# Kernel tuning notes

Measured on AMD Instinct MI355X. Metric: run time of the kernel, lower is better.

The kernel has to match this reference:

```python
import jax, jax.numpy as jnp
import numpy as np

H = 1024   # HIDDEN_DIM
V = 15000  # VOCAB_SIZE
L = 2      # NUM_LAYERS
E = 4      # experts per block
B, S = 32, 2048


def rmsnorm(x, w, eps=1e-6):
    return x * jax.lax.rsqrt(jnp.mean(x * x, axis=-1, keepdims=True) + eps) * w


def setup_inputs() -> dict:
    key = jax.random.key(0)
    ks = jax.random.split(key, 8)
    windows = jax.random.randint(ks[0], (B, S), 0, V, dtype=jnp.int32)
    hemis = jax.random.randint(ks[1], (B,), 0, 2, dtype=jnp.int32)
    experts = jax.random.randint(ks[2], (B,), 0, E, dtype=jnp.int32)
    emb = jax.random.normal(ks[3], (V, H), dtype=jnp.float32) * 0.02
    norm1_w = jnp.ones((L, H), dtype=jnp.float32)
    decay_logit = jnp.full((L, H), 2.0, dtype=jnp.float32)  # torch init: ones*2.0
    norm2_w = jnp.ones((L, H), dtype=jnp.float32)
    # expert weights, torch Linear layout [out, in] per expert: [L, E, H, H]
    Wexp = jax.random.normal(ks[4], (L, E, H, H), dtype=jnp.float32) * 0.02
    final_norm_w = jnp.ones((H,), dtype=jnp.float32)
    lm_head = jax.random.normal(ks[5], (V, H), dtype=jnp.float32) * 0.02
    return dict(windows=windows, hemis=hemis, experts=experts, emb=emb,
                norm1_w=norm1_w, decay_logit=decay_logit, norm2_w=norm2_w,
                Wexp=Wexp, final_norm_w=final_norm_w, lm_head=lm_head)


def reference(windows, hemis, experts, emb, norm1_w, decay_logit, norm2_w,
              Wexp, final_norm_w, lm_head):
    del hemis  # only used for router loss when targets are given (inference path)
    x = emb[windows]  # [B,S,H]
    onehot = jax.nn.one_hot(experts, E, dtype=x.dtype)  # [B,E]
    for l in range(L):
        xn = rmsnorm(x, norm1_w[l])
        decay = jax.nn.sigmoid(decay_logit[l])  # [H]

        def step(state, xt):
            s = state * decay + xt * (1.0 - decay)
            return s, s

        init = jnp.zeros((x.shape[0], H), dtype=x.dtype)
        _, states = jax.lax.scan(step, init, jnp.swapaxes(xn, 0, 1))  # [S,B,H]
        x = x + jnp.swapaxes(states, 0, 1)
        pool = rmsnorm(x, norm2_w[l])[:, -1, :]  # [B,H]
        # all 4 expert FFNs on the pooled state, then select by expert id
        out_all = jax.nn.relu(jnp.einsum('bh,edh->ebd', pool, Wexp[l]))  # [E,B,H]
        out = jnp.einsum('be,ebh->bh', onehot, out_all)  # [B,H]
        x = x + out[:, None, :]
    final_state = rmsnorm(x[:, -1, :], final_norm_w)
    logits = final_state @ lm_head.T  # [B,V]
    return logits
```

## Files before the change

### kernel.cpp

```cpp
#include <hip/hip_runtime.h>
#include <cstddef>
#include <cstdint>

#define H 1024
#define V 15000
#define NE 4
#define B 32
#define S 2048
#define EPS 1e-6f
#define CH 16
#define T0 128
#define NVB 469
#define LGRID 1024

typedef unsigned short u16;

__device__ __forceinline__ float wave_sum(float x) {
#pragma unroll
  for (int off = 32; off > 0; off >>= 1) x += __shfl_down(x, off);
  return x;
}

__device__ __forceinline__ float bf2f(u16 u) {
  union { uint32_t i; float f; } x;
  x.i = ((uint32_t)u) << 16;
  return x.f;
}

__device__ __forceinline__ u16 f2bf(float f) {
  union { float f; uint32_t i; } x;
  x.f = f;
  const uint32_t u = x.i;
  return (u16)((u + 0x7FFFu + ((u >> 16) & 1u)) >> 16);
}

__device__ __forceinline__ void pin4(float4& v) {
  asm volatile("" : "+v"(v.x), "+v"(v.y), "+v"(v.z), "+v"(v.w));
}

__global__ __launch_bounds__(256) void k_vocab(const float* __restrict__ emb,
                                               float* __restrict__ invr1,
                                               u16* __restrict__ embh) {
  const int gw = (blockIdx.x * blockDim.x + threadIdx.x) >> 6;
  const int lane = threadIdx.x & 63;
  if (gw >= V) return;
  const float4* row = (const float4*)(emb + (size_t)gw * H);
  float s = 0.f;
#pragma unroll
  for (int j = 0; j < 4; ++j) {
    const float4 f = row[lane + 64 * j];
    s += f.x * f.x + f.y * f.y + f.z * f.z + f.w * f.w;
    if (embh) {
      ushort4 h4;
      h4.x = f2bf(f.x); h4.y = f2bf(f.y); h4.z = f2bf(f.z); h4.w = f2bf(f.w);
      ((ushort4*)(embh + (size_t)gw * H))[lane + 64 * j] = h4;
    }
  }
  s = wave_sum(s);
  if (lane == 0) invr1[gw] = rsqrtf(s * (1.f / H) + EPS);
}

__global__ void k_bucket(const int* __restrict__ experts,
                         int* __restrict__ elist, int* __restrict__ ecnt) {
  if (threadIdx.x == 0 && blockIdx.x == 0) {
    int c[NE] = {0, 0, 0, 0};
    for (int b = 0; b < B; ++b) {
      const int e = experts[b];
      elist[e * B + c[e]] = b;
      c[e]++;
    }
    for (int e = 0; e < NE; ++e) ecnt[e] = c[e];
  }
}

template <int BF>
__global__ __launch_bounds__(1024, 8) void k_scanA(
    const int* __restrict__ windows, const float* __restrict__ emb,
    const u16* __restrict__ embh, const float* __restrict__ norm1_w,
    const float* __restrict__ decay_logit, const float* __restrict__ invr1,
    float* __restrict__ local1) {
  __shared__ int tok_l[T0];
  __shared__ float iv_l[T0];
  const int b = blockIdx.x / CH, c = blockIdx.x % CH;
  const int h = threadIdx.x;
  if (h < T0) {
    const int tok = windows[b * S + c * T0 + h];
    tok_l[h] = tok << 10;
    iv_l[h] = invr1[tok];
  }
  const float d1 = 1.f / (1.f + expf(-decay_logit[h]));
  const float gw = norm1_w[h] * (1.f - d1);
  __syncthreads();
  float s = 0.f;
  for (int t0 = 0; t0 < T0; t0 += 8) {
    float e[8], cv[8];
#pragma unroll
    for (int k = 0; k < 8; ++k) {
      if constexpr (BF)
        e[k] = bf2f(embh[(size_t)tok_l[t0 + k] + h]);
      else
        e[k] = emb[(size_t)tok_l[t0 + k] + h];
      cv[k] = iv_l[t0 + k] * gw;
    }
#pragma unroll
    for (int k = 0; k < 8; ++k) s = s * d1 + e[k] * cv[k];
  }
  local1[(size_t)(b * CH + c) * H + h] = s;
}

__global__ __launch_bounds__(1024) void k_scanB(
    const int* __restrict__ windows, const float* __restrict__ emb,
    const float* __restrict__ decay_logit, const float* __restrict__ local1,
    float* __restrict__ s1start, float* __restrict__ es1,
    float* __restrict__ invp) {
  __shared__ float red[16];
  const int b = blockIdx.x, h = threadIdx.x;
  const float d1 = 1.f / (1.f + expf(-decay_logit[h]));
  float dT = d1;
#pragma unroll
  for (int i = 0; i < 7; ++i) dT *= dT;
  float Sv = 0.f;
  for (int c = 0; c < CH; ++c) {
    const size_t idx = (size_t)(b * CH + c) * H + h;
    s1start[idx] = Sv;
    Sv = dT * Sv + local1[idx];
  }
  const int tl = windows[b * S + S - 1];
  const float v = emb[(size_t)tl * H + h] + Sv;
  es1[b * H + h] = v;
  const float q = wave_sum(v * v);
  if ((h & 63) == 0) red[h >> 6] = q;
  __syncthreads();
  if (h == 0) {
    float t = 0.f;
#pragma unroll
    for (int i = 0; i < 16; ++i) t += red[i];
    invp[b] = rsqrtf(t * (1.f / H) + EPS);
  }
}

__global__ __launch_bounds__(256) void k_expert2(
    const float* __restrict__ src, const float* __restrict__ invp,
    const float* __restrict__ n2w, const float* __restrict__ Wl,
    const int* __restrict__ elist, const int* __restrict__ ecnt,
    float* __restrict__ outp) {
  const int e = blockIdx.x >> 6;
  const int dgrp = blockIdx.x & 63;
  const int cnt = ecnt[e];
  if (cnt == 0) return;
  const int wave = threadIdx.x >> 6, lane = threadIdx.x & 63;
  const float* W = Wl + (size_t)e * H * H;
  const float4* n2w4 = (const float4*)n2w;
#pragma unroll 1
  for (int i = 0; i < 4; ++i) {
    const int dd = dgrp * 16 + wave * 4 + i;
    const float4* wr4 = (const float4*)(W + (size_t)dd * H);
    float4 w4[4];
#pragma unroll
    for (int j = 0; j < 4; ++j) w4[j] = wr4[lane + 64 * j];
#pragma unroll 1
    for (int bi = 0; bi < cnt; ++bi) {
      const int b = elist[e * B + bi];
      const float4* s4 = (const float4*)(src + b * H);
      float s = 0.f;
#pragma unroll
      for (int j = 0; j < 4; ++j) {
        const float4 sv = s4[lane + 64 * j];
        const float4 nv = n2w4[lane + 64 * j];
        s += w4[j].x * sv.x * nv.x + w4[j].y * sv.y * nv.y +
             w4[j].z * sv.z * nv.z + w4[j].w * sv.w * nv.w;
      }
      s = wave_sum(s);
      if (lane == 0) outp[b * H + dd] = fmaxf(s * invp[b], 0.f);
    }
  }
}

template <int BF>
__global__ __launch_bounds__(1024, 8) void k_fuseCD(
    const int* __restrict__ windows, const float* __restrict__ emb,
    const u16* __restrict__ embh, const float* __restrict__ norm1_w,
    const float* __restrict__ decay_logit, const float* __restrict__ invr1,
    const float* __restrict__ s1start, const float* __restrict__ out1,
    float* __restrict__ local2, float* __restrict__ x1last) {
  __shared__ int tok_l[T0];
  __shared__ float iv_l[T0];
  __shared__ float q[16 * H];
  __shared__ float rinv_l[16];
  const int b = blockIdx.x / CH, c = blockIdx.x % CH;
  const int h = threadIdx.x;
  if (h < T0) {
    const int tok = windows[b * S + c * T0 + h];
    tok_l[h] = tok << 10;
    iv_l[h] = invr1[tok];
  }
  const float d1 = 1.f / (1.f + expf(-decay_logit[h]));
  const float g1 = norm1_w[h] * (1.f - d1);
  const float d2 = 1.f / (1.f + expf(-decay_logit[H + h]));
  const float g2 = norm1_w[H + h] * (1.f - d2);
  const float o1 = out1[b * H + h];
  float s1 = s1start[(size_t)(b * CH + c) * H + h];
  __syncthreads();
  const int wv = h >> 6, lane = h & 63;
  float s2 = 0.f;
  for (int sb = 0; sb < T0 / 16; ++sb) {
#pragma unroll
    for (int g = 0; g < 2; ++g) {
      float e[8], cv[8];
#pragma unroll
      for (int k = 0; k < 8; ++k) {
        const int t = sb * 16 + g * 8 + k;
        if constexpr (BF)
          e[k] = bf2f(embh[(size_t)tok_l[t] + h]);
        else
          e[k] = emb[(size_t)tok_l[t] + h];
        cv[k] = iv_l[t] * g1;
      }
#pragma unroll
      for (int k = 0; k < 8; ++k) {
        s1 = s1 * d1 + e[k] * cv[k];
        q[(g * 8 + k) * H + h] = e[k] + s1 + o1;
      }
    }
    __syncthreads();
    const float4* q4 = (const float4*)(q + wv * H);
    float ssum = 0.f;
#pragma unroll
    for (int j = 0; j < 4; ++j) {
      const float4 f = q4[lane + 64 * j];
      ssum += f.x * f.x + f.y * f.y + f.z * f.z + f.w * f.w;
    }
    ssum = wave_sum(ssum);
    if (lane == 0) rinv_l[wv] = rsqrtf(ssum * (1.f / H) + EPS);
    __syncthreads();
#pragma unroll
    for (int g = 0; g < 2; ++g) {
      float xv[8], rc[8];
#pragma unroll
      for (int k = 0; k < 8; ++k) {
        xv[k] = q[(g * 8 + k) * H + h];
        rc[k] = rinv_l[g * 8 + k] * g2;
      }
#pragma unroll
      for (int k = 0; k < 8; ++k) s2 = s2 * d2 + xv[k] * rc[k];
    }
    __syncthreads();
  }
  local2[(size_t)(b * CH + c) * H + h] = s2;
  if (c == CH - 1) x1last[b * H + h] = q[15 * H + h];
}

__global__ __launch_bounds__(1024) void k_scanE(
    const float* __restrict__ decay_logit, const float* __restrict__ local2,
    const float* __restrict__ x1last, float* __restrict__ es2,
    float* __restrict__ invp) {
  __shared__ float red[16];
  const int b = blockIdx.x, h = threadIdx.x;
  const float d2 = 1.f / (1.f + expf(-decay_logit[H + h]));
  float dT = d2;
#pragma unroll
  for (int i = 0; i < 7; ++i) dT *= dT;
  float Sv = 0.f;
  for (int c = 0; c < CH; ++c)
    Sv = dT * Sv + local2[(size_t)(b * CH + c) * H + h];
  const float v = x1last[b * H + h] + Sv;
  es2[b * H + h] = v;
  const float q = wave_sum(v * v);
  if ((h & 63) == 0) red[h >> 6] = q;
  __syncthreads();
  if (h == 0) {
    float t = 0.f;
#pragma unroll
    for (int i = 0; i < 16; ++i) t += red[i];
    invp[32 + b] = rsqrtf(t * (1.f / H) + EPS);
  }
}

__global__ __launch_bounds__(256) void k_fstate(const float* __restrict__ es2,
    const float* __restrict__ out2, const float* __restrict__ fnw,
    float* __restrict__ fst) {
  __shared__ float red[4];
  const int b = blockIdx.x, tid = threadIdx.x;
  float4 x = ((const float4*)(es2 + b * H))[tid];
  const float4 y = ((const float4*)(out2 + b * H))[tid];
  x.x += y.x; x.y += y.y; x.z += y.z; x.w += y.w;
  float s = x.x * x.x + x.y * x.y + x.z * x.z + x.w * x.w;
  s = wave_sum(s);
  if ((tid & 63) == 0) red[tid >> 6] = s;
  __syncthreads();
  const float ir =
      rsqrtf((red[0] + red[1] + red[2] + red[3]) * (1.f / H) + EPS);
  const float4 w = ((const float4*)fnw)[tid];
  float4 o;
  o.x = x.x * ir * w.x; o.y = x.y * ir * w.y;
  o.z = x.z * ir * w.z; o.w = x.w * ir * w.w;
  ((float4*)(fst + b * H))[tid] = o;
}

__global__ __launch_bounds__(256, 4) void k_logits(const float* __restrict__ fst,
    const float* __restrict__ lm, float* __restrict__ part) {
  __shared__ float4 fs4[16 * 128];
  const int hh = blockIdx.x & 1;
  const int bgrp = (blockIdx.x >> 1) & 1;
  const int pblk = blockIdx.x >> 2;
  const int tid = threadIdx.x;
  const int wave = tid >> 6, lane = tid & 63;
  const int sg = lane >> 4;
  const int c = lane & 15;
  for (int j = tid; j < 16 * 128; j += 256) {
    const int bb = j >> 7, q = j & 127;
    fs4[j] = ((const float4*)fst)[(bgrp * 16 + bb) * 256 + hh * 128 + q];
  }
  __syncthreads();
  float* pdst = part + (size_t)hh * B * V + (size_t)bgrp * 16 * V;
#pragma unroll 1
  for (int vblk = pblk; vblk < NVB; vblk += LGRID / 4) {
    const int v0 = vblk * 32 + wave * 8 + sg * 2;
    float4 rv[2][8];
#pragma unroll
    for (int i = 0; i < 2; ++i) {
      int r = v0 + i;
      if (r > V - 1) r = V - 1;
      const float4* rp = (const float4*)(lm + (size_t)r * H) + hh * 128 + c;
#pragma unroll
      for (int jj = 0; jj < 8; ++jj) rv[i][jj] = rp[16 * jj];
    }
#pragma unroll
    for (int i = 0; i < 2; ++i)
#pragma unroll
      for (int jj = 0; jj < 8; ++jj) pin4(rv[i][jj]);
    float acc[2][16];
#pragma unroll
    for (int i = 0; i < 2; ++i)
#pragma unroll
      for (int bb = 0; bb < 16; ++bb) acc[i][bb] = 0.f;
#pragma unroll
    for (int jj = 0; jj < 8; ++jj) {
      const int hoff = c + 16 * jj;
#pragma unroll
      for (int bb = 0; bb < 16; ++bb) {
        const float4 fv = fs4[bb * 128 + hoff];
#pragma unroll
        for (int i = 0; i < 2; ++i) {
          acc[i][bb] += rv[i][jj].x * fv.x + rv[i][jj].y * fv.y +
                        rv[i][jj].z * fv.z + rv[i][jj].w * fv.w;
        }
      }
    }
#pragma unroll
    for (int off = 1; off < 16; off <<= 1)
#pragma unroll
      for (int i = 0; i < 2; ++i)
#pragma unroll
        for (int bb = 0; bb < 16; ++bb)
          acc[i][bb] += __shfl_xor(acc[i][bb], off);
    if (c == 0) {
#pragma unroll
      for (int bb = 0; bb < 16; ++bb)
#pragma unroll
        for (int i = 0; i < 2; ++i) {
          const int r = v0 + i;
          if (r < V) pdst[(size_t)bb * V + r] = acc[i][bb];
        }
    }
  }
}

__global__ __launch_bounds__(256) void k_comb(const float* __restrict__ part,
                                              float* __restrict__ outp) {
  const int i = blockIdx.x * 256 + threadIdx.x;
  if (i < B * V) outp[i] = part[i] + part[B * V + i];
}

extern "C" void kernel_launch(void* const* d_in, const int* in_sizes, int n_in,
                              void* d_out, int out_size, void* d_ws,
                              size_t ws_size, hipStream_t stream) {
  const int* windows = (const int*)d_in[0];
  const int* experts = (const int*)d_in[2];
  const float* emb = (const float*)d_in[3];
  const float* norm1_w = (const float*)d_in[4];
  const float* decay_logit = (const float*)d_in[5];
  const float* norm2_w = (const float*)d_in[6];
  const float* Wexp = (const float*)d_in[7];
  const float* final_norm_w = (const float*)d_in[8];
  const float* lm_head = (const float*)d_in[9];
  float* outp = (float*)d_out;

  float* ws = (float*)d_ws;
  float* invr1 = ws;
  float* local1 = invr1 + 15360;
  float* s1start = local1 + B * CH * H;
  float* local2 = s1start + B * CH * H;
  float* out1 = local2 + B * CH * H;
  float* out2 = out1 + B * H;
  float* es1 = out2 + B * H;
  float* es2 = es1 + B * H;
  float* x1last = es2 + B * H;
  float* fst = x1last + B * H;
  float* invp = fst + B * H;
  int* elist = (int*)(invp + 64);
  int* ecnt = elist + NE * B;
  float* part = local1;
  u16* embh = (u16*)(((uintptr_t)(ecnt + NE) + 255) & ~(uintptr_t)255);
  const size_t need = (size_t)((char*)embh - (char*)d_ws) + (size_t)V * H * 2;
  const bool use_bf = ws_size >= need;

  k_vocab<<<(V * 64 + 255) / 256, 256, 0, stream>>>(emb, invr1,
                                                    use_bf ? embh : nullptr);
  k_bucket<<<1, 64, 0, stream>>>(experts, elist, ecnt);
  if (use_bf)
    k_scanA<1><<<B * CH, 1024, 0, stream>>>(windows, emb, embh, norm1_w,
                                            decay_logit, invr1, local1);
  else
    k_scanA<0><<<B * CH, 1024, 0, stream>>>(windows, emb, embh, norm1_w,
                                            decay_logit, invr1, local1);
  k_scanB<<<B, 1024, 0, stream>>>(windows, emb, decay_logit, local1, s1start,
                                  es1, invp);
  k_expert2<<<NE * 64, 256, 0, stream>>>(es1, invp, norm2_w, Wexp, elist,
                                         ecnt, out1);
  if (use_bf)
    k_fuseCD<1><<<B * CH, 1024, 0, stream>>>(windows, emb, embh, norm1_w,
                                             decay_logit, invr1, s1start,
                                             out1, local2, x1last);
  else
    k_fuseCD<0><<<B * CH, 1024, 0, stream>>>(windows, emb, embh, norm1_w,
                                             decay_logit, invr1, s1start,
                                             out1, local2, x1last);
  k_scanE<<<B, 1024, 0, stream>>>(decay_logit, local2, x1last, es2, invp);
  k_expert2<<<NE * 64, 256, 0, stream>>>(es2, invp + 32, norm2_w + H,
                                         Wexp + (size_t)NE * H * H, elist,
                                         ecnt, out2);
  k_fstate<<<B, 256, 0, stream>>>(es2, out2, final_norm_w, fst);
  k_logits<<<LGRID, 256, 0, stream>>>(fst, lm_head, part);
  k_comb<<<(B * V + 255) / 256, 256, 0, stream>>>(part, outp);
}
```

Before: 323.4 us.

## Use 512-thread two-channel scan blocks with finer sequence chunks and register-held norms

The chunked scan kernels now give each thread two adjacent hidden channels, loaded as one 32-bit bf16 pair or a float2, and run 512 threads per block. The sequence is cut into 32 chunks of 64 tokens instead of 16 chunks of 128, so the grid doubles and each block's serial scan halves, with the decay-power exponent in the carry kernels adjusted to match. In the fused kernel the per-token values stay in registers and only per-thread squared sums go through a small shared buffer for the RMS reduction, replacing the full 16xH shared tile and one barrier per sub-block. The aims are wider loads, less shared-memory traffic and more parallelism; the cost is more chunk-carry work in the serial combine kernels and more register pressure per thread.

```diff
diff --git a/kernel.cpp b/kernel.cpp
--- a/kernel.cpp
+++ b/kernel.cpp
@@ -8,8 +8,9 @@
 #define B 32
 #define S 2048
 #define EPS 1e-6f
-#define CH 16
-#define T0 128
+#define CH 32
+#define T0 64
+#define SB 8
 #define NVB 469
 #define LGRID 1024
 
@@ -24,6 +25,17 @@
 __device__ __forceinline__ float bf2f(u16 u) {
   union { uint32_t i; float f; } x;
   x.i = ((uint32_t)u) << 16;
+  return x.f;
+}
+
+__device__ __forceinline__ float bflo(uint32_t u) {
+  union { uint32_t i; float f; } x;
+  x.i = u << 16;
+  return x.f;
+}
+__device__ __forceinline__ float bfhi(uint32_t u) {
+  union { uint32_t i; float f; } x;
+  x.i = u & 0xFFFF0000u;
   return x.f;
 }
 
@@ -74,7 +86,7 @@
 }
 
 template <int BF>
-__global__ __launch_bounds__(1024, 8) void k_scanA(
+__global__ __launch_bounds__(512, 8) void k_scanA(
     const int* __restrict__ windows, const float* __restrict__ emb,
     const u16* __restrict__ embh, const float* __restrict__ norm1_w,
     const float* __restrict__ decay_logit, const float* __restrict__ invr1,
@@ -82,30 +94,39 @@
   __shared__ int tok_l[T0];
   __shared__ float iv_l[T0];
   const int b = blockIdx.x / CH, c = blockIdx.x % CH;
-  const int h = threadIdx.x;
-  if (h < T0) {
-    const int tok = windows[b * S + c * T0 + h];
-    tok_l[h] = tok << 10;
-    iv_l[h] = invr1[tok];
-  }
-  const float d1 = 1.f / (1.f + expf(-decay_logit[h]));
-  const float gw = norm1_w[h] * (1.f - d1);
-  __syncthreads();
-  float s = 0.f;
-  for (int t0 = 0; t0 < T0; t0 += 8) {
-    float e[8], cv[8];
-#pragma unroll
-    for (int k = 0; k < 8; ++k) {
+  const int tid = threadIdx.x;
+  const int h2 = tid * 2;
+  if (tid < T0) {
+    const int tok = windows[b * S + c * T0 + tid];
+    tok_l[tid] = tok << 10;
+    iv_l[tid] = invr1[tok];
+  }
+  const float d1a = 1.f / (1.f + expf(-decay_logit[h2]));
+  const float d1b = 1.f / (1.f + expf(-decay_logit[h2 + 1]));
+  const float g1a = norm1_w[h2] * (1.f - d1a);
+  const float g1b = norm1_w[h2 + 1] * (1.f - d1b);
+  __syncthreads();
+  float sa = 0.f, sbv = 0.f;
+  for (int t0 = 0; t0 < T0; t0 += SB) {
+    uint32_t u[SB];
+    float2 ef[SB];
+#pragma unroll
+    for (int k = 0; k < SB; ++k) {
       if constexpr (BF)
-        e[k] = bf2f(embh[(size_t)tok_l[t0 + k] + h]);
+        u[k] = *(const uint32_t*)(embh + (size_t)(tok_l[t0 + k] + h2));
       else
-        e[k] = emb[(size_t)tok_l[t0 + k] + h];
-      cv[k] = iv_l[t0 + k] * gw;
-    }
-#pragma unroll
-    for (int k = 0; k < 8; ++k) s = s * d1 + e[k] * cv[k];
-  }
-  local1[(size_t)(b * CH + c) * H + h] = s;
+        ef[k] = *(const float2*)(emb + (size_t)(tok_l[t0 + k] + h2));
+    }
+#pragma unroll
+    for (int k = 0; k < SB; ++k) {
+      const float iv = iv_l[t0 + k];
+      const float ea = BF ? bflo(u[k]) : ef[k].x;
+      const float eb = BF ? bfhi(u[k]) : ef[k].y;
+      sa = sa * d1a + ea * (iv * g1a);
+      sbv = sbv * d1b + eb * (iv * g1b);
+    }
+  }
+  *(float2*)(local1 + (size_t)(b * CH + c) * H + h2) = make_float2(sa, sbv);
 }
 
 __global__ __launch_bounds__(1024) void k_scanB(
@@ -118,7 +139,7 @@
   const float d1 = 1.f / (1.f + expf(-decay_logit[h]));
   float dT = d1;
 #pragma unroll
-  for (int i = 0; i < 7; ++i) dT *= dT;
+  for (int i = 0; i < 6; ++i) dT *= dT;
   float Sv = 0.f;
   for (int c = 0; c < CH; ++c) {
     const size_t idx = (size_t)(b * CH + c) * H + h;
@@ -177,7 +198,7 @@
 }
 
 template <int BF>
-__global__ __launch_bounds__(1024, 8) void k_fuseCD(
+__global__ __launch_bounds__(512, 8) void k_fuseCD(
     const int* __restrict__ windows, const float* __restrict__ emb,
     const u16* __restrict__ embh, const float* __restrict__ norm1_w,
     const float* __restrict__ decay_logit, const float* __restrict__ invr1,
@@ -185,69 +206,70 @@
     float* __restrict__ local2, float* __restrict__ x1last) {
   __shared__ int tok_l[T0];
   __shared__ float iv_l[T0];
-  __shared__ float q[16 * H];
-  __shared__ float rinv_l[16];
+  __shared__ float sq[SB][512];
+  __shared__ float rinv_l[SB];
   const int b = blockIdx.x / CH, c = blockIdx.x % CH;
-  const int h = threadIdx.x;
-  if (h < T0) {
-    const int tok = windows[b * S + c * T0 + h];
-    tok_l[h] = tok << 10;
-    iv_l[h] = invr1[tok];
-  }
-  const float d1 = 1.f / (1.f + expf(-decay_logit[h]));
-  const float g1 = norm1_w[h] * (1.f - d1);
-  const float d2 = 1.f / (1.f + expf(-decay_logit[H + h]));
-  const float g2 = norm1_w[H + h] * (1.f - d2);
-  const float o1 = out1[b * H + h];
-  float s1 = s1start[(size_t)(b * CH + c) * H + h];
-  __syncthreads();
-  const int wv = h >> 6, lane = h & 63;
-  float s2 = 0.f;
-  for (int sb = 0; sb < T0 / 16; ++sb) {
-#pragma unroll
-    for (int g = 0; g < 2; ++g) {
-      float e[8], cv[8];
-#pragma unroll
-      for (int k = 0; k < 8; ++k) {
-        const int t = sb * 16 + g * 8 + k;
-        if constexpr (BF)
-          e[k] = bf2f(embh[(size_t)tok_l[t] + h]);
-        else
-          e[k] = emb[(size_t)tok_l[t] + h];
-        cv[k] = iv_l[t] * g1;
-      }
-#pragma unroll
-      for (int k = 0; k < 8; ++k) {
-        s1 = s1 * d1 + e[k] * cv[k];
-        q[(g * 8 + k) * H + h] = e[k] + s1 + o1;
-      }
+  const int tid = threadIdx.x;
+  const int h2 = 2 * tid;
+  if (tid < T0) {
+    const int tok = windows[b * S + c * T0 + tid];
+    tok_l[tid] = tok << 10;
+    iv_l[tid] = invr1[tok];
+  }
+  const float d1a = 1.f / (1.f + expf(-decay_logit[h2]));
+  const float d1b = 1.f / (1.f + expf(-decay_logit[h2 + 1]));
+  const float g1a = norm1_w[h2] * (1.f - d1a);
+  const float g1b = norm1_w[h2 + 1] * (1.f - d1b);
+  const float d2a = 1.f / (1.f + expf(-decay_logit[H + h2]));
+  const float d2b = 1.f / (1.f + expf(-decay_logit[H + h2 + 1]));
+  const float g2a = norm1_w[H + h2] * (1.f - d2a);
+  const float g2b = norm1_w[H + h2 + 1] * (1.f - d2b);
+  const float2 o1 = *(const float2*)(out1 + b * H + h2);
+  const float2 s1v = *(const float2*)(s1start + (size_t)(b * CH + c) * H + h2);
+  float s1a = s1v.x, s1b = s1v.y;
+  float s2a = 0.f, s2b = 0.f;
+  __syncthreads();
+  const int wv = tid >> 6, lane = tid & 63;
+  float x1a[SB], x1b[SB];
+  for (int sb = 0; sb < T0 / SB; ++sb) {
+    uint32_t u[SB];
+    float2 ef[SB];
+#pragma unroll
+    for (int k = 0; k < SB; ++k) {
+      const int t = sb * SB + k;
+      if constexpr (BF)
+        u[k] = *(const uint32_t*)(embh + (size_t)(tok_l[t] + h2));
+      else
+        ef[k] = *(const float2*)(emb + (size_t)(tok_l[t] + h2));
+    }
+#pragma unroll
+    for (int k = 0; k < SB; ++k) {
+      const float iv = iv_l[sb * SB + k];
+      const float ea = BF ? bflo(u[k]) : ef[k].x;
+      const float eb = BF ? bfhi(u[k]) : ef[k].y;
+      s1a = s1a * d1a + ea * (iv * g1a);
+      s1b = s1b * d1b + eb * (iv * g1b);
+      x1a[k] = ea + s1a + o1.x;
+      x1b[k] = eb + s1b + o1.y;
+      sq[k][tid] = x1a[k] * x1a[k] + x1b[k] * x1b[k];
     }
     __syncthreads();
-    const float4* q4 = (const float4*)(q + wv * H);
     float ssum = 0.f;
 #pragma unroll
-    for (int j = 0; j < 4; ++j) {
-      const float4 f = q4[lane + 64 * j];
-      ssum += f.x * f.x + f.y * f.y + f.z * f.z + f.w * f.w;
-    }
+    for (int j = 0; j < 8; ++j) ssum += sq[wv][lane + 64 * j];
     ssum = wave_sum(ssum);
     if (lane == 0) rinv_l[wv] = rsqrtf(ssum * (1.f / H) + EPS);
     __syncthreads();
 #pragma unroll
-    for (int g = 0; g < 2; ++g) {
-      float xv[8], rc[8];
-#pragma unroll
-      for (int k = 0; k < 8; ++k) {
-        xv[k] = q[(g * 8 + k) * H + h];
-        rc[k] = rinv_l[g * 8 + k] * g2;
-      }
-#pragma unroll
-      for (int k = 0; k < 8; ++k) s2 = s2 * d2 + xv[k] * rc[k];
-    }
-    __syncthreads();
-  }
-  local2[(size_t)(b * CH + c) * H + h] = s2;
-  if (c == CH - 1) x1last[b * H + h] = q[15 * H + h];
+    for (int k = 0; k < SB; ++k) {
+      const float ra = rinv_l[k];
+      s2a = s2a * d2a + x1a[k] * (ra * g2a);
+      s2b = s2b * d2b + x1b[k] * (ra * g2b);
+    }
+  }
+  *(float2*)(local2 + (size_t)(b * CH + c) * H + h2) = make_float2(s2a, s2b);
+  if (c == CH - 1)
+    *(float2*)(x1last + b * H + h2) = make_float2(x1a[SB - 1], x1b[SB - 1]);
 }
 
 __global__ __launch_bounds__(1024) void k_scanE(
@@ -259,7 +281,7 @@
   const float d2 = 1.f / (1.f + expf(-decay_logit[H + h]));
   float dT = d2;
 #pragma unroll
-  for (int i = 0; i < 7; ++i) dT *= dT;
+  for (int i = 0; i < 6; ++i) dT *= dT;
   float Sv = 0.f;
   for (int c = 0; c < CH; ++c)
     Sv = dT * Sv + local2[(size_t)(b * CH + c) * H + h];
@@ -409,23 +431,23 @@
                                                     use_bf ? embh : nullptr);
   k_bucket<<<1, 64, 0, stream>>>(experts, elist, ecnt);
   if (use_bf)
-    k_scanA<1><<<B * CH, 1024, 0, stream>>>(windows, emb, embh, norm1_w,
-                                            decay_logit, invr1, local1);
+    k_scanA<1><<<B * CH, 512, 0, stream>>>(windows, emb, embh, norm1_w,
+                                           decay_logit, invr1, local1);
   else
-    k_scanA<0><<<B * CH, 1024, 0, stream>>>(windows, emb, embh, norm1_w,
-                                            decay_logit, invr1, local1);
+    k_scanA<0><<<B * CH, 512, 0, stream>>>(windows, emb, embh, norm1_w,
+                                           decay_logit, invr1, local1);
   k_scanB<<<B, 1024, 0, stream>>>(windows, emb, decay_logit, local1, s1start,
                                   es1, invp);
   k_expert2<<<NE * 64, 256, 0, stream>>>(es1, invp, norm2_w, Wexp, elist,
                                          ecnt, out1);
   if (use_bf)
-    k_fuseCD<1><<<B * CH, 1024, 0, stream>>>(windows, emb, embh, norm1_w,
-                                             decay_logit, invr1, s1start,
-                                             out1, local2, x1last);
+    k_fuseCD<1><<<B * CH, 512, 0, stream>>>(windows, emb, embh, norm1_w,
+                                            decay_logit, invr1, s1start,
+                                            out1, local2, x1last);
   else
-    k_fuseCD<0><<<B * CH, 1024, 0, stream>>>(windows, emb, embh, norm1_w,
-                                             decay_logit, invr1, s1start,
-                                             out1, local2, x1last);
+    k_fuseCD<0><<<B * CH, 512, 0, stream>>>(windows, emb, embh, norm1_w,
+                                            decay_logit, invr1, s1start,
+                                            out1, local2, x1last);
   k_scanE<<<B, 1024, 0, stream>>>(decay_logit, local2, x1last, es2, invp);
   k_expert2<<<NE * 64, 256, 0, stream>>>(es2, invp + 32, norm2_w + H,
                                          Wexp + (size_t)NE * H * H, elist,
```

New measurement: 302.2 us. 6.6% less time.
